# Kernel optimization log

Measured on AMD Instinct MI355X. Metric: run time of the kernel, lower is better.

Reference implementation:

```python
import jax, jax.numpy as jnp
import numpy as np

NUM_BINS = 10
NUM_CLASSES = 128
ALPHA = 0.999
LABEL_SMOOTHING = 0.0


def setup_inputs() -> dict:
    key = jax.random.key(0)
    k1, k2, k3 = jax.random.split(key, 3)
    B, T, C = 16, 4096, NUM_CLASSES
    return {
        "pred_logits": jax.random.normal(k1, (B, T, C), dtype=jnp.float32),
        "target_prob": jax.random.uniform(k2, (B, T, C), dtype=jnp.float32),
        "mask": jax.random.uniform(k3, (B, T, 1), dtype=jnp.float32),
        "GD_stat_ema": jnp.ones((NUM_BINS,), dtype=jnp.float32),
        "label_stat_ema_each_class": jnp.ones((NUM_CLASSES * 3,), dtype=jnp.float32),
    }


def _bce_with_logits(x, t):
    # numerically stable BCEWithLogitsLoss, reduction='none'
    return jnp.maximum(x, 0.0) - x * t + jnp.log1p(jnp.exp(-jnp.abs(x)))


def _update_ema(ema, hist, num_bins):
    hist = hist / jnp.maximum(hist.sum(), 1e-10) * num_bins
    ema = ema * ALPHA + (1.0 - ALPHA) * hist
    return ema / jnp.maximum(ema.sum(), 1e-10) * num_bins


def reference(pred_logits, target_prob, mask, GD_stat_ema, label_stat_ema_each_class):
    m = jnp.broadcast_to(mask, pred_logits.shape)
    tp = jnp.clip(target_prob, LABEL_SMOOTHING, 1.0 - LABEL_SMOOTHING)

    raw_loss = _bce_with_logits(pred_logits, tp)
    pred_prob = jax.nn.sigmoid(pred_logits)
    grad_mag = jnp.abs(pred_prob - tp)

    bin_idx = jnp.clip(jnp.floor(grad_mag * NUM_BINS).astype(jnp.int32), 0, NUM_BINS - 1)
    GD_weights = 1.0 / jax.lax.stop_gradient(GD_stat_ema[bin_idx])

    # per-class 3-way probability bin: idx in [0, 3*num_classes)
    tpi = jnp.clip(jnp.floor(tp * 3.0).astype(jnp.int32), 0, 2) + 3 * jnp.arange(NUM_CLASSES, dtype=jnp.int32)
    classes_weights = 1.0 / jax.lax.stop_gradient(label_stat_ema_each_class[tpi])

    weights = jnp.sqrt(GD_weights * classes_weights)
    loss = (raw_loss * weights * m).sum() / jnp.maximum(m.sum(), 1e-10)

    # weighted histograms (bincount with float weights)
    GD_hist = jnp.zeros((NUM_BINS,), dtype=jnp.float32).at[bin_idx.ravel()].add(m.ravel())
    label_hist = jnp.zeros((NUM_CLASSES * 3,), dtype=jnp.float32).at[tpi.ravel()].add(m.ravel())

    GD_ema_new = _update_ema(GD_stat_ema, GD_hist, NUM_BINS)
    label_ema_new = _update_ema(label_stat_ema_each_class, label_hist, NUM_CLASSES * 3)
    return loss, GD_ema_new, label_ema_new
```

## Files before the change

### kernel.cpp

```cpp
#include <hip/hip_runtime.h>

#define NBINS 10
#define LBINS 384
#define NOUT  395
#define PSTRIDE 400
#define PQ (PSTRIDE / 4)
#define BLOCK 256

#define SGRID 1024
#define OUTER 2
#define BATCH 4
#define SGSTR (SGRID * BLOCK)

__global__ __launch_bounds__(256) void ghm_main_s(
    const float* __restrict__ xg, const float* __restrict__ tg,
    const float* __restrict__ mask,
    const float* __restrict__ gd_ema, const float* __restrict__ lab_ema,
    float* __restrict__ ws)
{
    __shared__ float s_rsgd[NBINS];
    __shared__ float s_rslab[LBINS];
    __shared__ float s_out[PSTRIDE];
    __shared__ float s_red[4];

    const int tid = threadIdx.x;
    if (tid < NBINS) s_rsgd[tid] = __builtin_amdgcn_rsqf(gd_ema[tid]);
    for (int i = tid; i < LBINS; i += BLOCK) s_rslab[i] = __builtin_amdgcn_rsqf(lab_ema[i]);
    for (int i = tid; i < PSTRIDE; i += BLOCK) s_out[i] = 0.f;
    __syncthreads();

    const int c0 = (tid & 31) * 4;
    float wl[4][3];
#pragma unroll
    for (int j = 0; j < 4; ++j)
#pragma unroll
        for (int t = 0; t < 3; ++t) wl[j][t] = s_rslab[(c0 + j) * 3 + t];

    float lab[4][3] = {{0.f}};
    float gdl[NBINS];
#pragma unroll
    for (int b = 0; b < NBINS; ++b) gdl[b] = 0.f;
    float loss_acc = 0.f;

    const float4* x4 = (const float4*)xg;
    const float4* t4 = (const float4*)tg;
    const int i0 = blockIdx.x * BLOCK + tid;

#pragma unroll
    for (int o = 0; o < OUTER; ++o) {
        float4 xv[BATCH], tv[BATCH]; float mv[BATCH];
#pragma unroll
        for (int k = 0; k < BATCH; ++k) {
            const int i = i0 + (o * BATCH + k) * SGSTR;
            xv[k] = x4[i];
            tv[k] = t4[i];
            mv[k] = mask[i >> 5];
        }
#pragma unroll
        for (int k = 0; k < BATCH; ++k) {
            const float m = mv[k];
            const float xs[4] = {xv[k].x, xv[k].y, xv[k].z, xv[k].w};
            const float ts[4] = {tv[k].x, tv[k].y, tv[k].z, tv[k].w};
            unsigned pack = 0u;
#pragma unroll
            for (int j = 0; j < 4; ++j) {
                const float x  = xs[j];
                const float tp = ts[j];
                const float E  = __expf(-fabsf(x));
                const float z  = 1.f + E;
                const float raw = fmaxf(x, 0.f) - x * tp + __logf(z);
                const float inv = __builtin_amdgcn_rcpf(z);
                const float tps = (x >= 0.f) ? tp : 1.f - tp;
                const float g   = fabsf(inv - tps);
                int bin = (int)(g * 10.f);  bin = bin > 9 ? 9 : bin;
                int t3  = (int)(tp * 3.f);  t3  = t3 > 2 ? 2 : t3;
                const float wlj = (t3 == 0) ? wl[j][0] : ((t3 == 1) ? wl[j][1] : wl[j][2]);
                const float w = s_rsgd[bin] * wlj;
                loss_acc = fmaf(raw * m, w, loss_acc);
#pragma unroll
                for (int t = 0; t < 3; ++t) lab[j][t] += (t3 == t) ? m : 0.f;
                pack += 1u << (3 * bin);
            }
#pragma unroll
            for (int b = 0; b < NBINS; ++b)
                gdl[b] = fmaf(m, (float)((pack >> (3 * b)) & 7u), gdl[b]);
        }
    }

    const int lane = tid & 63, wv = tid >> 6;
    float v = loss_acc;
#pragma unroll
    for (int off = 32; off > 0; off >>= 1) v += __shfl_down(v, off);
    if (lane == 0) s_red[wv] = v;
#pragma unroll
    for (int b = 0; b < NBINS; ++b) {
        float g = gdl[b];
#pragma unroll
        for (int off = 32; off > 0; off >>= 1) g += __shfl_down(g, off);
        if (lane == 0) atomicAdd(&s_out[1 + b], g);
    }
#pragma unroll
    for (int j = 0; j < 4; ++j)
#pragma unroll
        for (int t = 0; t < 3; ++t)
            atomicAdd(&s_out[11 + (c0 + j) * 3 + t], lab[j][t]);
    __syncthreads();

    float* slot = ws + (size_t)blockIdx.x * PSTRIDE;
    if (tid == 0) slot[0] = s_red[0] + s_red[1] + s_red[2] + s_red[3];
    if (tid >= 1) slot[tid] = s_out[tid];
    if (tid < PSTRIDE - BLOCK) slot[BLOCK + tid] = s_out[BLOCK + tid];
}

__global__ __launch_bounds__(256) void ghm_fin1(
    const float* __restrict__ ws, float* __restrict__ ws2)
{
    __shared__ float4 r[BLOCK];
    const int tid = threadIdx.x;
    const float4* p = (const float4*)ws + blockIdx.x;
    float4 a = make_float4(0.f, 0.f, 0.f, 0.f);
    for (int b = tid; b < SGRID; b += BLOCK) {
        float4 u = p[(size_t)b * PQ];
        a.x += u.x; a.y += u.y; a.z += u.z; a.w += u.w;
    }
    r[tid] = a;
    __syncthreads();
    for (int off = BLOCK / 2; off > 0; off >>= 1) {
        if (tid < off) {
            float4 u = r[tid + off];
            r[tid].x += u.x; r[tid].y += u.y; r[tid].z += u.z; r[tid].w += u.w;
        }
        __syncthreads();
    }
    if (tid == 0) ((float4*)ws2)[blockIdx.x] = r[0];
}

__global__ __launch_bounds__(512) void ghm_fin2(
    const float* __restrict__ sv_g,
    const float* __restrict__ gd_ema, const float* __restrict__ lab_ema,
    float* __restrict__ out)
{
    __shared__ float sv[PSTRIDE];
    __shared__ float red[512];
    __shared__ float s_sc[1];

    const int tid = threadIdx.x;
    if (tid < PSTRIDE) sv[tid] = sv_g[tid];
    __syncthreads();

    if (tid == 0) {
        float ms = 0.f;
        for (int b = 0; b < NBINS; ++b) ms += sv[1 + b];
        const float inv_m = 1.f / fmaxf(ms, 1e-10f);
        s_sc[0] = inv_m;
        out[0] = sv[0] * inv_m;
        float ge[NBINS], gs = 0.f;
        for (int b = 0; b < NBINS; ++b) {
            ge[b] = gd_ema[b] * 0.999f + 0.001f * (sv[1 + b] * inv_m * (float)NBINS);
            gs += ge[b];
        }
        const float ig = 1.f / fmaxf(gs, 1e-10f);
        for (int b = 0; b < NBINS; ++b) out[1 + b] = ge[b] * ig * (float)NBINS;
    }
    __syncthreads();
    const float inv_m = s_sc[0];

    float e = 0.f;
    if (tid < LBINS)
        e = lab_ema[tid] * 0.999f + 0.001f * (sv[11 + tid] * inv_m * (float)LBINS);
    red[tid] = e;
    __syncthreads();
    for (int off = 256; off > 0; off >>= 1) {
        if (tid < off) red[tid] += red[tid + off];
        __syncthreads();
    }
    const float ie = (float)LBINS / fmaxf(red[0], 1e-10f);
    if (tid < LBINS) out[11 + tid] = e * ie;
}

#define NSLICE 8
#define SLICE_STRIDE 512
#define AGRID 2048
#define AITER 4
#define AGSTR (AGRID * BLOCK)

__global__ __launch_bounds__(256, 3) void ghm_main_a(
    const float* __restrict__ xg, const float* __restrict__ tg,
    const float* __restrict__ mask,
    const float* __restrict__ gd_ema, const float* __restrict__ lab_ema,
    float* __restrict__ ws)
{
    __shared__ float s_rsgd[NBINS];
    __shared__ float s_rslab[LBINS];
    __shared__ float s_hlab[LBINS];
    __shared__ float s_hgd[NBINS];
    __shared__ float s_red[4];

    const int tid = threadIdx.x;
    if (tid < NBINS) { s_rsgd[tid] = __builtin_amdgcn_rsqf(gd_ema[tid]); s_hgd[tid] = 0.f; }
    for (int i = tid; i < LBINS; i += BLOCK) {
        s_rslab[i] = __builtin_amdgcn_rsqf(lab_ema[i]);
        s_hlab[i]  = 0.f;
    }
    __syncthreads();

    const int c0 = (tid & 31) * 4;
    float wl[4][3];
#pragma unroll
    for (int j = 0; j < 4; ++j)
#pragma unroll
        for (int t = 0; t < 3; ++t) wl[j][t] = s_rslab[(c0 + j) * 3 + t];

    float lab[4][3] = {{0.f}};
    float gdl[NBINS];
#pragma unroll
    for (int b = 0; b < NBINS; ++b) gdl[b] = 0.f;
    float loss_acc = 0.f;

    const float4* x4 = (const float4*)xg;
    const float4* t4 = (const float4*)tg;
    const int i0 = blockIdx.x * BLOCK + tid;

    float4 xv[AITER], tv[AITER]; float mv[AITER];
#pragma unroll
    for (int k = 0; k < AITER; ++k) {
        const int i = i0 + k * AGSTR;
        xv[k] = x4[i]; tv[k] = t4[i]; mv[k] = mask[i >> 5];
    }
#pragma unroll
    for (int k = 0; k < AITER; ++k) {
        const float m = mv[k];
        const float xs[4] = {xv[k].x, xv[k].y, xv[k].z, xv[k].w};
        const float ts[4] = {tv[k].x, tv[k].y, tv[k].z, tv[k].w};
        unsigned pack = 0u;
#pragma unroll
        for (int j = 0; j < 4; ++j) {
            const float x  = xs[j];
            const float tp = ts[j];
            const float E  = __expf(-fabsf(x));
            const float z  = 1.f + E;
            const float raw = fmaxf(x, 0.f) - x * tp + __logf(z);
            const float inv = __builtin_amdgcn_rcpf(z);
            const float tps = (x >= 0.f) ? tp : 1.f - tp;
            const float g   = fabsf(inv - tps);
            int bin = (int)(g * 10.f);  bin = bin > 9 ? 9 : bin;
            int t3  = (int)(tp * 3.f);  t3  = t3 > 2 ? 2 : t3;
            const float wlj = (t3 == 0) ? wl[j][0] : ((t3 == 1) ? wl[j][1] : wl[j][2]);
            const float w = s_rsgd[bin] * wlj;
            loss_acc = fmaf(raw * m, w, loss_acc);
#pragma unroll
            for (int t = 0; t < 3; ++t) lab[j][t] += (t3 == t) ? m : 0.f;
            pack += 1u << (3 * bin);
        }
#pragma unroll
        for (int b = 0; b < NBINS; ++b)
            gdl[b] = fmaf(m, (float)((pack >> (3 * b)) & 7u), gdl[b]);
    }

    const int lane = tid & 63, wv = tid >> 6;
    float v = loss_acc;
#pragma unroll
    for (int off = 32; off > 0; off >>= 1) v += __shfl_down(v, off);
    if (lane == 0) s_red[wv] = v;
#pragma unroll
    for (int b = 0; b < NBINS; ++b) {
        float g = gdl[b];
#pragma unroll
        for (int off = 32; off > 0; off >>= 1) g += __shfl_down(g, off);
        if (lane == 0) atomicAdd(&s_hgd[b], g);
    }
#pragma unroll
    for (int j = 0; j < 4; ++j)
#pragma unroll
        for (int t = 0; t < 3; ++t)
            atomicAdd(&s_hlab[(c0 + j) * 3 + t], lab[j][t]);
    __syncthreads();

    float* wss = ws + (blockIdx.x & (NSLICE - 1)) * SLICE_STRIDE;
    if (tid == 0) atomicAdd(&wss[0], s_red[0] + s_red[1] + s_red[2] + s_red[3]);
    if (tid < NBINS) atomicAdd(&wss[1 + tid], s_hgd[tid]);
    for (int e = tid; e < LBINS; e += BLOCK) atomicAdd(&wss[1 + NBINS + e], s_hlab[e]);
}

__global__ __launch_bounds__(512) void ghm_fin_a(
    const float* __restrict__ ws,
    const float* __restrict__ gd_ema, const float* __restrict__ lab_ema,
    float* __restrict__ out)
{
    __shared__ float red[512];
    __shared__ float s_gde[NBINS];
    __shared__ float s_gesum;

    const int tid = threadIdx.x;
    float v = 0.f;
    if (tid < NOUT) {
#pragma unroll
        for (int s = 0; s < NSLICE; ++s) v += ws[s * SLICE_STRIDE + tid];
    }
    red[tid] = (tid >= 1 && tid < 1 + NBINS) ? v : 0.f;
    __syncthreads();
    for (int off = 256; off > 0; off >>= 1) {
        if (tid < off) red[tid] += red[tid + off];
        __syncthreads();
    }
    const float msum = red[0];
    __syncthreads();
    const float inv_m = 1.f / fmaxf(msum, 1e-10f);
    if (tid == 0) out[0] = v * inv_m;
    if (tid >= 1 && tid < 1 + NBINS) {
        float hn = v * inv_m * (float)NBINS;
        s_gde[tid - 1] = gd_ema[tid - 1] * 0.999f + 0.001f * hn;
    }
    __syncthreads();
    if (tid == 0) {
        float s = 0.f;
        for (int b = 0; b < NBINS; ++b) s += s_gde[b];
        s_gesum = s;
    }
    __syncthreads();
    if (tid >= 1 && tid < 1 + NBINS)
        out[tid] = s_gde[tid - 1] / fmaxf(s_gesum, 1e-10f) * (float)NBINS;

    float e = 0.f;
    if (tid >= 1 + NBINS && tid < NOUT) {
        float hn = v * inv_m * (float)LBINS;
        e = lab_ema[tid - 1 - NBINS] * 0.999f + 0.001f * hn;
    }
    red[tid] = e;
    __syncthreads();
    for (int off = 256; off > 0; off >>= 1) {
        if (tid < off) red[tid] += red[tid + off];
        __syncthreads();
    }
    const float esum = red[0];
    if (tid >= 1 + NBINS && tid < NOUT)
        out[tid] = e / fmaxf(esum, 1e-10f) * (float)LBINS;
}

extern "C" void kernel_launch(void* const* d_in, const int* in_sizes, int n_in,
                              void* d_out, int out_size, void* d_ws, size_t ws_size,
                              hipStream_t stream)
{
    const float* logits  = (const float*)d_in[0];
    const float* tprob   = (const float*)d_in[1];
    const float* mask    = (const float*)d_in[2];
    const float* gd_ema  = (const float*)d_in[3];
    const float* lab_ema = (const float*)d_in[4];
    float* out = (float*)d_out;
    float* ws  = (float*)d_ws;

    const size_t need = ((size_t)SGRID * PSTRIDE + PSTRIDE) * sizeof(float);
    if (ws_size >= need) {
        float* ws2 = ws + (size_t)SGRID * PSTRIDE;
        ghm_main_s<<<SGRID, BLOCK, 0, stream>>>(logits, tprob, mask, gd_ema, lab_ema, ws);
        ghm_fin1<<<PQ, BLOCK, 0, stream>>>(ws, ws2);
        ghm_fin2<<<1, 512, 0, stream>>>(ws2, gd_ema, lab_ema, out);
    } else {
        hipMemsetAsync(ws, 0, NSLICE * SLICE_STRIDE * sizeof(float), stream);
        ghm_main_a<<<AGRID, BLOCK, 0, stream>>>(logits, tprob, mask, gd_ema, lab_ema, ws);
        ghm_fin_a<<<1, 512, 0, stream>>>(ws, gd_ema, lab_ema, out);
    }
}
```

Before: 136.1 us.

## Stream inputs through LDS ring buffer with async global_load_lds in ghm_main_s

Replaces the two batched register loads in the sliced main kernel with an 8-stage pipeline that moves x and target data straight from global memory into a 4-slot LDS ring using global_load_lds. Explicit vmcnt waits keep up to three stages in flight while the current one is computed. The aim is to cut register pressure and keep more memory requests outstanding to hide HBM latency. In exchange the kernel uses about 32KB of extra LDS per block, which can lower occupancy, and it relies on hand-written waitcnt ordering.

```diff
diff --git a/kernel.cpp b/kernel.cpp
--- a/kernel.cpp
+++ b/kernel.cpp
@@ -8,9 +8,13 @@
 #define BLOCK 256
 
 #define SGRID 1024
-#define OUTER 2
-#define BATCH 4
+#define NSTAGE 8
+#define RING 4
 #define SGSTR (SGRID * BLOCK)
+
+#define GLDS16(gp, lp) __builtin_amdgcn_global_load_lds(                      \
+    (const __attribute__((address_space(1))) void*)(const void*)(gp),          \
+    (__attribute__((address_space(3))) void*)(void*)(lp), 16, 0, 0)
 
 __global__ __launch_bounds__(256) void ghm_main_s(
     const float* __restrict__ xg, const float* __restrict__ tg,
@@ -22,6 +26,8 @@
     __shared__ float s_rslab[LBINS];
     __shared__ float s_out[PSTRIDE];
     __shared__ float s_red[4];
+    __shared__ float4 sx[RING][BLOCK];
+    __shared__ float4 st[RING][BLOCK];
 
     const int tid = threadIdx.x;
     if (tid < NBINS) s_rsgd[tid] = __builtin_amdgcn_rsqf(gd_ema[tid]);
@@ -46,192 +52,39 @@
     const float4* t4 = (const float4*)tg;
     const int i0 = blockIdx.x * BLOCK + tid;
 
-#pragma unroll
-    for (int o = 0; o < OUTER; ++o) {
-        float4 xv[BATCH], tv[BATCH]; float mv[BATCH];
-#pragma unroll
-        for (int k = 0; k < BATCH; ++k) {
-            const int i = i0 + (o * BATCH + k) * SGSTR;
-            xv[k] = x4[i];
-            tv[k] = t4[i];
-            mv[k] = mask[i >> 5];
-        }
-#pragma unroll
-        for (int k = 0; k < BATCH; ++k) {
-            const float m = mv[k];
-            const float xs[4] = {xv[k].x, xv[k].y, xv[k].z, xv[k].w};
-            const float ts[4] = {tv[k].x, tv[k].y, tv[k].z, tv[k].w};
-            unsigned pack = 0u;
-#pragma unroll
-            for (int j = 0; j < 4; ++j) {
-                const float x  = xs[j];
-                const float tp = ts[j];
-                const float E  = __expf(-fabsf(x));
-                const float z  = 1.f + E;
-                const float raw = fmaxf(x, 0.f) - x * tp + __logf(z);
-                const float inv = __builtin_amdgcn_rcpf(z);
-                const float tps = (x >= 0.f) ? tp : 1.f - tp;
-                const float g   = fabsf(inv - tps);
-                int bin = (int)(g * 10.f);  bin = bin > 9 ? 9 : bin;
-                int t3  = (int)(tp * 3.f);  t3  = t3 > 2 ? 2 : t3;
-                const float wlj = (t3 == 0) ? wl[j][0] : ((t3 == 1) ? wl[j][1] : wl[j][2]);
-                const float w = s_rsgd[bin] * wlj;
-                loss_acc = fmaf(raw * m, w, loss_acc);
-#pragma unroll
-                for (int t = 0; t < 3; ++t) lab[j][t] += (t3 == t) ? m : 0.f;
-                pack += 1u << (3 * bin);
-            }
-#pragma unroll
-            for (int b = 0; b < NBINS; ++b)
-                gdl[b] = fmaf(m, (float)((pack >> (3 * b)) & 7u), gdl[b]);
-        }
-    }
-
-    const int lane = tid & 63, wv = tid >> 6;
-    float v = loss_acc;
-#pragma unroll
-    for (int off = 32; off > 0; off >>= 1) v += __shfl_down(v, off);
-    if (lane == 0) s_red[wv] = v;
-#pragma unroll
-    for (int b = 0; b < NBINS; ++b) {
-        float g = gdl[b];
-#pragma unroll
-        for (int off = 32; off > 0; off >>= 1) g += __shfl_down(g, off);
-        if (lane == 0) atomicAdd(&s_out[1 + b], g);
-    }
-#pragma unroll
-    for (int j = 0; j < 4; ++j)
-#pragma unroll
-        for (int t = 0; t < 3; ++t)
-            atomicAdd(&s_out[11 + (c0 + j) * 3 + t], lab[j][t]);
-    __syncthreads();
-
-    float* slot = ws + (size_t)blockIdx.x * PSTRIDE;
-    if (tid == 0) slot[0] = s_red[0] + s_red[1] + s_red[2] + s_red[3];
-    if (tid >= 1) slot[tid] = s_out[tid];
-    if (tid < PSTRIDE - BLOCK) slot[BLOCK + tid] = s_out[BLOCK + tid];
-}
-
-__global__ __launch_bounds__(256) void ghm_fin1(
-    const float* __restrict__ ws, float* __restrict__ ws2)
-{
-    __shared__ float4 r[BLOCK];
-    const int tid = threadIdx.x;
-    const float4* p = (const float4*)ws + blockIdx.x;
-    float4 a = make_float4(0.f, 0.f, 0.f, 0.f);
-    for (int b = tid; b < SGRID; b += BLOCK) {
-        float4 u = p[(size_t)b * PQ];
-        a.x += u.x; a.y += u.y; a.z += u.z; a.w += u.w;
-    }
-    r[tid] = a;
-    __syncthreads();
-    for (int off = BLOCK / 2; off > 0; off >>= 1) {
-        if (tid < off) {
-            float4 u = r[tid + off];
-            r[tid].x += u.x; r[tid].y += u.y; r[tid].z += u.z; r[tid].w += u.w;
-        }
-        __syncthreads();
-    }
-    if (tid == 0) ((float4*)ws2)[blockIdx.x] = r[0];
-}
-
-__global__ __launch_bounds__(512) void ghm_fin2(
-    const float* __restrict__ sv_g,
-    const float* __restrict__ gd_ema, const float* __restrict__ lab_ema,
-    float* __restrict__ out)
-{
-    __shared__ float sv[PSTRIDE];
-    __shared__ float red[512];
-    __shared__ float s_sc[1];
-
-    const int tid = threadIdx.x;
-    if (tid < PSTRIDE) sv[tid] = sv_g[tid];
-    __syncthreads();
-
-    if (tid == 0) {
-        float ms = 0.f;
-        for (int b = 0; b < NBINS; ++b) ms += sv[1 + b];
-        const float inv_m = 1.f / fmaxf(ms, 1e-10f);
-        s_sc[0] = inv_m;
-        out[0] = sv[0] * inv_m;
-        float ge[NBINS], gs = 0.f;
-        for (int b = 0; b < NBINS; ++b) {
-            ge[b] = gd_ema[b] * 0.999f + 0.001f * (sv[1 + b] * inv_m * (float)NBINS);
-            gs += ge[b];
-        }
-        const float ig = 1.f / fmaxf(gs, 1e-10f);
-        for (int b = 0; b < NBINS; ++b) out[1 + b] = ge[b] * ig * (float)NBINS;
-    }
-    __syncthreads();
-    const float inv_m = s_sc[0];
-
-    float e = 0.f;
-    if (tid < LBINS)
-        e = lab_ema[tid] * 0.999f + 0.001f * (sv[11 + tid] * inv_m * (float)LBINS);
-    red[tid] = e;
-    __syncthreads();
-    for (int off = 256; off > 0; off >>= 1) {
-        if (tid < off) red[tid] += red[tid + off];
-        __syncthreads();
-    }
-    const float ie = (float)LBINS / fmaxf(red[0], 1e-10f);
-    if (tid < LBINS) out[11 + tid] = e * ie;
-}
-
-#define NSLICE 8
-#define SLICE_STRIDE 512
-#define AGRID 2048
-#define AITER 4
-#define AGSTR (AGRID * BLOCK)
-
-__global__ __launch_bounds__(256, 3) void ghm_main_a(
-    const float* __restrict__ xg, const float* __restrict__ tg,
-    const float* __restrict__ mask,
-    const float* __restrict__ gd_ema, const float* __restrict__ lab_ema,
-    float* __restrict__ ws)
-{
-    __shared__ float s_rsgd[NBINS];
-    __shared__ float s_rslab[LBINS];
-    __shared__ float s_hlab[LBINS];
-    __shared__ float s_hgd[NBINS];
-    __shared__ float s_red[4];
-
-    const int tid = threadIdx.x;
-    if (tid < NBINS) { s_rsgd[tid] = __builtin_amdgcn_rsqf(gd_ema[tid]); s_hgd[tid] = 0.f; }
-    for (int i = tid; i < LBINS; i += BLOCK) {
-        s_rslab[i] = __builtin_amdgcn_rsqf(lab_ema[i]);
-        s_hlab[i]  = 0.f;
-    }
-    __syncthreads();
-
-    const int c0 = (tid & 31) * 4;
-    float wl[4][3];
-#pragma unroll
-    for (int j = 0; j < 4; ++j)
-#pragma unroll
-        for (int t = 0; t < 3; ++t) wl[j][t] = s_rslab[(c0 + j) * 3 + t];
-
-    float lab[4][3] = {{0.f}};
-    float gdl[NBINS];
-#pragma unroll
-    for (int b = 0; b < NBINS; ++b) gdl[b] = 0.f;
-    float loss_acc = 0.f;
-
-    const float4* x4 = (const float4*)xg;
-    const float4* t4 = (const float4*)tg;
-    const int i0 = blockIdx.x * BLOCK + tid;
-
-    float4 xv[AITER], tv[AITER]; float mv[AITER];
-#pragma unroll
-    for (int k = 0; k < AITER; ++k) {
-        const int i = i0 + k * AGSTR;
-        xv[k] = x4[i]; tv[k] = t4[i]; mv[k] = mask[i >> 5];
-    }
-#pragma unroll
-    for (int k = 0; k < AITER; ++k) {
+    float mv[NSTAGE];
+#pragma unroll
+    for (int k = 0; k < NSTAGE; ++k) mv[k] = mask[(i0 + k * SGSTR) >> 5];
+    asm volatile("s_waitcnt vmcnt(0)" ::: "memory");
+
+#pragma unroll
+    for (int k = 0; k < RING; ++k) {
+        const int i = i0 + k * SGSTR;
+        GLDS16(x4 + i, &sx[k][tid]);
+        GLDS16(t4 + i, &st[k][tid]);
+    }
+
+#pragma unroll
+    for (int k = 0; k < NSTAGE; ++k) {
+        if (k <= NSTAGE - RING)          asm volatile("s_waitcnt vmcnt(6)" ::: "memory");
+        else if (k == NSTAGE - RING + 1) asm volatile("s_waitcnt vmcnt(4)" ::: "memory");
+        else if (k == NSTAGE - RING + 2) asm volatile("s_waitcnt vmcnt(2)" ::: "memory");
+        else                             asm volatile("s_waitcnt vmcnt(0)" ::: "memory");
+
+        const int r = k & (RING - 1);
+        const float4 xv = sx[r][tid];
+        const float4 tv = st[r][tid];
+
+        if (k + RING < NSTAGE) {
+            asm volatile("s_waitcnt lgkmcnt(0)" ::: "memory");
+            const int i = i0 + (k + RING) * SGSTR;
+            GLDS16(x4 + i, &sx[r][tid]);
+            GLDS16(t4 + i, &st[r][tid]);
+        }
+
         const float m = mv[k];
-        const float xs[4] = {xv[k].x, xv[k].y, xv[k].z, xv[k].w};
-        const float ts[4] = {tv[k].x, tv[k].y, tv[k].z, tv[k].w};
+        const float xs[4] = {xv.x, xv.y, xv.z, xv.w};
+        const float ts[4] = {tv.x, tv.y, tv.z, tv.w};
         unsigned pack = 0u;
 #pragma unroll
         for (int j = 0; j < 4; ++j) {
@@ -267,6 +120,176 @@
         float g = gdl[b];
 #pragma unroll
         for (int off = 32; off > 0; off >>= 1) g += __shfl_down(g, off);
+        if (lane == 0) atomicAdd(&s_out[1 + b], g);
+    }
+#pragma unroll
+    for (int j = 0; j < 4; ++j)
+#pragma unroll
+        for (int t = 0; t < 3; ++t)
+            atomicAdd(&s_out[11 + (c0 + j) * 3 + t], lab[j][t]);
+    __syncthreads();
+
+    float* slot = ws + (size_t)blockIdx.x * PSTRIDE;
+    if (tid == 0) slot[0] = s_red[0] + s_red[1] + s_red[2] + s_red[3];
+    if (tid >= 1) slot[tid] = s_out[tid];
+    if (tid < PSTRIDE - BLOCK) slot[BLOCK + tid] = s_out[BLOCK + tid];
+}
+
+__global__ __launch_bounds__(256) void ghm_fin1(
+    const float* __restrict__ ws, float* __restrict__ ws2)
+{
+    __shared__ float4 r[BLOCK];
+    const int tid = threadIdx.x;
+    const float4* p = (const float4*)ws + blockIdx.x;
+    float4 a = make_float4(0.f, 0.f, 0.f, 0.f);
+    for (int b = tid; b < SGRID; b += BLOCK) {
+        float4 u = p[(size_t)b * PQ];
+        a.x += u.x; a.y += u.y; a.z += u.z; a.w += u.w;
+    }
+    r[tid] = a;
+    __syncthreads();
+    for (int off = BLOCK / 2; off > 0; off >>= 1) {
+        if (tid < off) {
+            float4 u = r[tid + off];
+            r[tid].x += u.x; r[tid].y += u.y; r[tid].z += u.z; r[tid].w += u.w;
+        }
+        __syncthreads();
+    }
+    if (tid == 0) ((float4*)ws2)[blockIdx.x] = r[0];
+}
+
+__global__ __launch_bounds__(512) void ghm_fin2(
+    const float* __restrict__ sv_g,
+    const float* __restrict__ gd_ema, const float* __restrict__ lab_ema,
+    float* __restrict__ out)
+{
+    __shared__ float sv[PSTRIDE];
+    __shared__ float red[512];
+    __shared__ float s_sc[1];
+
+    const int tid = threadIdx.x;
+    if (tid < PSTRIDE) sv[tid] = sv_g[tid];
+    __syncthreads();
+
+    if (tid == 0) {
+        float ms = 0.f;
+        for (int b = 0; b < NBINS; ++b) ms += sv[1 + b];
+        const float inv_m = 1.f / fmaxf(ms, 1e-10f);
+        s_sc[0] = inv_m;
+        out[0] = sv[0] * inv_m;
+        float ge[NBINS], gs = 0.f;
+        for (int b = 0; b < NBINS; ++b) {
+            ge[b] = gd_ema[b] * 0.999f + 0.001f * (sv[1 + b] * inv_m * (float)NBINS);
+            gs += ge[b];
+        }
+        const float ig = 1.f / fmaxf(gs, 1e-10f);
+        for (int b = 0; b < NBINS; ++b) out[1 + b] = ge[b] * ig * (float)NBINS;
+    }
+    __syncthreads();
+    const float inv_m = s_sc[0];
+
+    float e = 0.f;
+    if (tid < LBINS)
+        e = lab_ema[tid] * 0.999f + 0.001f * (sv[11 + tid] * inv_m * (float)LBINS);
+    red[tid] = e;
+    __syncthreads();
+    for (int off = 256; off > 0; off >>= 1) {
+        if (tid < off) red[tid] += red[tid + off];
+        __syncthreads();
+    }
+    const float ie = (float)LBINS / fmaxf(red[0], 1e-10f);
+    if (tid < LBINS) out[11 + tid] = e * ie;
+}
+
+#define NSLICE 8
+#define SLICE_STRIDE 512
+#define AGRID 2048
+#define AITER 4
+#define AGSTR (AGRID * BLOCK)
+
+__global__ __launch_bounds__(256, 3) void ghm_main_a(
+    const float* __restrict__ xg, const float* __restrict__ tg,
+    const float* __restrict__ mask,
+    const float* __restrict__ gd_ema, const float* __restrict__ lab_ema,
+    float* __restrict__ ws)
+{
+    __shared__ float s_rsgd[NBINS];
+    __shared__ float s_rslab[LBINS];
+    __shared__ float s_hlab[LBINS];
+    __shared__ float s_hgd[NBINS];
+    __shared__ float s_red[4];
+
+    const int tid = threadIdx.x;
+    if (tid < NBINS) { s_rsgd[tid] = __builtin_amdgcn_rsqf(gd_ema[tid]); s_hgd[tid] = 0.f; }
+    for (int i = tid; i < LBINS; i += BLOCK) {
+        s_rslab[i] = __builtin_amdgcn_rsqf(lab_ema[i]);
+        s_hlab[i]  = 0.f;
+    }
+    __syncthreads();
+
+    const int c0 = (tid & 31) * 4;
+    float wl[4][3];
+#pragma unroll
+    for (int j = 0; j < 4; ++j)
+#pragma unroll
+        for (int t = 0; t < 3; ++t) wl[j][t] = s_rslab[(c0 + j) * 3 + t];
+
+    float lab[4][3] = {{0.f}};
+    float gdl[NBINS];
+#pragma unroll
+    for (int b = 0; b < NBINS; ++b) gdl[b] = 0.f;
+    float loss_acc = 0.f;
+
+    const float4* x4 = (const float4*)xg;
+    const float4* t4 = (const float4*)tg;
+    const int i0 = blockIdx.x * BLOCK + tid;
+
+    float4 xv[AITER], tv[AITER]; float mv[AITER];
+#pragma unroll
+    for (int k = 0; k < AITER; ++k) {
+        const int i = i0 + k * AGSTR;
+        xv[k] = x4[i]; tv[k] = t4[i]; mv[k] = mask[i >> 5];
+    }
+#pragma unroll
+    for (int k = 0; k < AITER; ++k) {
+        const float m = mv[k];
+        const float xs[4] = {xv[k].x, xv[k].y, xv[k].z, xv[k].w};
+        const float ts[4] = {tv[k].x, tv[k].y, tv[k].z, tv[k].w};
+        unsigned pack = 0u;
+#pragma unroll
+        for (int j = 0; j < 4; ++j) {
+            const float x  = xs[j];
+            const float tp = ts[j];
+            const float E  = __expf(-fabsf(x));
+            const float z  = 1.f + E;
+            const float raw = fmaxf(x, 0.f) - x * tp + __logf(z);
+            const float inv = __builtin_amdgcn_rcpf(z);
+            const float tps = (x >= 0.f) ? tp : 1.f - tp;
+            const float g   = fabsf(inv - tps);
+            int bin = (int)(g * 10.f);  bin = bin > 9 ? 9 : bin;
+            int t3  = (int)(tp * 3.f);  t3  = t3 > 2 ? 2 : t3;
+            const float wlj = (t3 == 0) ? wl[j][0] : ((t3 == 1) ? wl[j][1] : wl[j][2]);
+            const float w = s_rsgd[bin] * wlj;
+            loss_acc = fmaf(raw * m, w, loss_acc);
+#pragma unroll
+            for (int t = 0; t < 3; ++t) lab[j][t] += (t3 == t) ? m : 0.f;
+            pack += 1u << (3 * bin);
+        }
+#pragma unroll
+        for (int b = 0; b < NBINS; ++b)
+            gdl[b] = fmaf(m, (float)((pack >> (3 * b)) & 7u), gdl[b]);
+    }
+
+    const int lane = tid & 63, wv = tid >> 6;
+    float v = loss_acc;
+#pragma unroll
+    for (int off = 32; off > 0; off >>= 1) v += __shfl_down(v, off);
+    if (lane == 0) s_red[wv] = v;
+#pragma unroll
+    for (int b = 0; b < NBINS; ++b) {
+        float g = gdl[b];
+#pragma unroll
+        for (int off = 32; off > 0; off >>= 1) g += __shfl_down(g, off);
         if (lane == 0) atomicAdd(&s_hgd[b], g);
     }
 #pragma unroll
```

New measurement: 138.9 us. 2.1% more time.
